# Kernel tuning notes

Measured on AMD Instinct MI355X. Metric: run time of the kernel, lower is better.

Reference implementation:

```python
import jax, jax.numpy as jnp
import numpy as np


def _relu(x):
    return jnp.maximum(x, 0.0)


def _wn(V, g):
    # torch weight_norm with dim=None: W = g * V / ||V||_F (scalar g)
    return g * V / jnp.linalg.norm(V)


def _wn_rank(V, g):
    # V: [rank, out, in], g: [rank] -> per-rank weight-normed weights
    n = jnp.sqrt(jnp.sum(V * V, axis=(1, 2), keepdims=True))
    return g[:, None, None] * V / n


def setup_inputs() -> dict:
    key = jax.random.key(0)
    ks = jax.random.split(key, 20)
    B, N, D, H, R, HK, G = 16, 64, 512, 512, 8, 64, 2
    f = lambda i, shape, s=1.0: jax.random.normal(ks[i], shape, dtype=jnp.float32) * s
    u = lambda i, shape: jax.random.uniform(ks[i], shape, dtype=jnp.float32)
    return {
        'v': f(0, (B, N, D)), 'q': f(1, (B, N, D)), 'a': f(2, (B, N, D)),
        'V_v': f(3, (H, D), 0.05), 'g_v': u(4, (1,)), 'b_v': f(5, (H,), 0.05),
        'V_q': f(6, (H, D), 0.05), 'g_q': u(7, (1,)), 'b_q': f(8, (H,), 0.05),
        'V_a': f(9, (H, D), 0.05), 'g_a': u(10, (1,)), 'b_a': f(11, (H,), 0.05),
        'Vn_v': f(12, (R, HK, H), 0.05), 'gn_v': u(13, (R,)), 'bn_v': f(14, (R, HK), 0.05),
        'Vn_qa': f(15, (R, HK, H), 0.05), 'gn_qa': u(16, (R,)), 'bn_qa': f(17, (R, HK), 0.05),
        'T_g': f(18, (R, HK, HK, HK, G), 0.02),  # T_g with h_out=1 squeezed
        'gamma': u(19, (H,)), 'beta': jnp.zeros((H,), jnp.float32),
    }


def reference(v, q, a, V_v, g_v, b_v, V_q, g_q, b_q, V_a, g_a, b_a,
              Vn_v, gn_v, bn_v, Vn_qa, gn_qa, bn_qa, T_g, gamma, beta):
    # Tucker projections (FCNet = weight-normed Linear + ReLU; dropout off in eval)
    v_t = _relu(v @ _wn(V_v, g_v).T + b_v)  # [B, Nv, H]
    q_t = _relu(q @ _wn(V_q, g_q).T + b_q)  # [B, Nq, H]
    a_t = _relu(a @ _wn(V_a, g_a).T + b_a)  # [B, Na, H]

    # Per-rank FCNets, vectorized over the rank loop (q_net and a_net share weights)
    Wv = _wn_rank(Vn_v, gn_v)    # [R, HK, H]
    Wqa = _wn_rank(Vn_qa, gn_qa)  # [R, HK, H]
    v_r = _relu(jnp.einsum('bnh,rkh->brnk', v_t, Wv) + bn_v[None, :, None, :])   # [B,R,Nv,HK]
    q_r = _relu(jnp.einsum('bnh,rkh->brnk', q_t, Wqa) + bn_qa[None, :, None, :])  # [B,R,Nq,HK]
    a_r = _relu(jnp.einsum('bnh,rkh->brnk', a_t, Wqa) + bn_qa[None, :, None, :])  # [B,R,Na,HK]

    # ModeProduct summed over rank: f_emb[b,v,q,m,g] = sum_r T_g[r,h,k,l,g] v_r q_r a_r
    t = jnp.einsum('brvh,rhklg->brvklg', v_r, T_g)
    t = jnp.einsum('brvklg,brqk->brvqlg', t, q_r)
    f_emb = jnp.einsum('brvqlg,brml->bvqmg', t, a_r)  # [B, Nv, Nq, Na, G]

    # logits = einsum('bdv,bvqag,bdqi,bdaj->bdijg').sum(-1).squeeze(3).squeeze(2)
    # with i=j=1 this is: logits[b,d] = sum_{v,q,a,g} v_t f_emb q_t a_t
    t2 = jnp.einsum('bvqag,bad->bvqdg', f_emb, a_t)
    t2 = jnp.einsum('bvqdg,bqd->bvdg', t2, q_t)
    logits = jnp.einsum('bvdg,bvd->bd', t2, v_t)  # [B, H]

    # BatchNorm1d (training-mode batch statistics, eps=1e-5)
    mu = jnp.mean(logits, axis=0)
    var = jnp.var(logits, axis=0)
    logits = (logits - mu) / jnp.sqrt(var + 1e-5) * gamma + beta

    # torch returns f_emb.squeeze(4): no-op since glimpse=2
    return f_emb, logits
```

## Files before the change

### kernel.cpp

```cpp
#include <hip/hip_runtime.h>
#include <hip/hip_fp16.h>
#include <math.h>


typedef _Float16 f16x8 __attribute__((ext_vector_type(8)));
typedef float f32x4 __attribute__((ext_vector_type(4)));

__device__ __forceinline__ unsigned short f2h(float x) {
  _Float16 h = (_Float16)x;
  return __builtin_bit_cast(unsigned short, h);
}

__device__ __forceinline__ int fragoff(int row, int kr) {
  return (((row & 15) + (((kr >> 2) & 3) << 4)) << 3) + (kr & 3) + (((kr >> 4) & 1) << 2);
}

#define WS_NRM 0
#define WS_VT  32
#define WS_QT  (WS_VT + 524288)
#define WS_AT  (WS_QT + 524288)
#define WS_LP  (WS_AT + 524288)
#define WS_LR  (WS_LP + 524288)
#define WS_PRT (WS_LR + 8192)
#define WS_H   (WS_PRT + 1280)
#define H_VRL 0
#define H_QR2 524288
#define H_AR2 1048576
#define H_T2  1572864
#define H_AT16 5767168
#define H_IN16 6291456
#define H_WB16 7864320
#define H_WN16 8650752
#define H_RP16 9175040

__global__ __launch_bounds__(256) void k_norms_part(
    const float* __restrict__ Vv, const float* __restrict__ Vq, const float* __restrict__ Va,
    const float* __restrict__ Vnv, const float* __restrict__ Vnqa, float* __restrict__ prt)
{
  const int bx = blockIdx.x;
  int n, j;
  const float* base;
  if (bx < 192) {
    n = bx >> 6; j = bx & 63;
    base = (n == 0 ? Vv : n == 1 ? Vq : Va) + j * 4096;
  } else {
    int t = bx - 192;
    n = 3 + (t >> 3); j = t & 7;
    base = (n < 11 ? Vnv + (n - 3) * 32768 : Vnqa + (n - 11) * 32768) + j * 4096;
  }
  const float4* p4 = (const float4*)base;
  float s = 0.f;
  #pragma unroll
  for (int i = 0; i < 4; ++i) {
    float4 x = p4[threadIdx.x + i * 256];
    s += x.x * x.x + x.y * x.y + x.z * x.z + x.w * x.w;
  }
  __shared__ float red[256];
  red[threadIdx.x] = s; __syncthreads();
  for (int off = 128; off > 0; off >>= 1) {
    if (threadIdx.x < off) red[threadIdx.x] += red[threadIdx.x + off];
    __syncthreads();
  }
  if (threadIdx.x == 0) prt[n * 64 + j] = red[0];
}

__global__ __launch_bounds__(64) void k_norms_fin(const float* __restrict__ prt, float* __restrict__ wsn)
{
  const int n = blockIdx.x, t = threadIdx.x;
  const int cnt = (n < 3) ? 64 : 8;
  float s = (t < cnt) ? prt[n * 64 + t] : 0.f;
  #pragma unroll
  for (int off = 32; off > 0; off >>= 1) s += __shfl_down(s, off);
  if (t == 0) wsn[n] = sqrtf(s);
}

__global__ __launch_bounds__(256) void k_inconv16(
    const float* __restrict__ v, const float* __restrict__ q, const float* __restrict__ a,
    unsigned short* __restrict__ IN16)
{
  const int z = blockIdx.y;
  const float4* src = (const float4*)((z == 0) ? v : (z == 1) ? q : a);
  #pragma unroll
  for (int i = 0; i < 8; ++i) {
    int f = blockIdx.x * 2048 + threadIdx.x + i * 256;
    int row = f >> 7, d0 = (f & 127) * 4;
    float4 x = src[f];
    ushort4 pk;
    pk.x = f2h(x.x); pk.y = f2h(x.y); pk.z = f2h(x.z); pk.w = f2h(x.w);
    int lanep = (row & 15) + (((d0 >> 2) & 3) << 4);
    int jb = ((d0 >> 4) & 1) << 2;
    size_t off = ((size_t)(z * 64 + (row >> 4)) * 16 + (d0 >> 5)) * 512 + lanep * 8 + jb;
    *(ushort4*)&IN16[off] = pk;
  }
}

__global__ __launch_bounds__(256) void k_wconv16(
    const float* __restrict__ Wv, const float* __restrict__ Wq, const float* __restrict__ Wa,
    const float* __restrict__ gv, const float* __restrict__ gq, const float* __restrict__ ga,
    const float* __restrict__ wsn, unsigned short* __restrict__ WB16)
{
  const int z = blockIdx.y;
  const float4* src = (const float4*)((z == 0) ? Wv : (z == 1) ? Wq : Wa);
  const float scale = ((z == 0) ? gv[0] : (z == 1) ? gq[0] : ga[0]) / wsn[z];
  #pragma unroll
  for (int i = 0; i < 8; ++i) {
    int f = blockIdx.x * 2048 + threadIdx.x + i * 256;
    int n = f >> 7, d0 = (f & 127) * 4;
    float4 x = src[f];
    ushort4 pk;
    pk.x = f2h(x.x * scale); pk.y = f2h(x.y * scale);
    pk.z = f2h(x.z * scale); pk.w = f2h(x.w * scale);
    int lanep = (n & 15) + (((d0 >> 2) & 3) << 4);
    int jb = ((d0 >> 4) & 1) << 2;
    size_t off = ((size_t)(z * 32 + (n >> 4)) * 16 + (d0 >> 5)) * 512 + lanep * 8 + jb;
    *(ushort4*)&WB16[off] = pk;
  }
}

__global__ __launch_bounds__(256) void k_wnconv16(
    const float* __restrict__ Vnv, const float* __restrict__ Vnqa,
    const float* __restrict__ gnv, const float* __restrict__ gnqa,
    const float* __restrict__ wsn, unsigned short* __restrict__ WN16)
{
  const int zr = blockIdx.x >> 2, sub = blockIdx.x & 3;
  const int zq = zr >> 3, r = zr & 7;
  const float4* src = (const float4*)((zq == 0 ? Vnv : Vnqa) + (size_t)r * 32768);
  const float scale = (zq == 0) ? (gnv[r] / wsn[3 + r]) : (gnqa[r] / wsn[11 + r]);
  #pragma unroll
  for (int i = 0; i < 8; ++i) {
    int f = sub * 2048 + threadIdx.x + i * 256;
    int n = f >> 7, d0 = (f & 127) * 4;
    float4 x = src[f];
    ushort4 pk;
    pk.x = f2h(x.x * scale); pk.y = f2h(x.y * scale);
    pk.z = f2h(x.z * scale); pk.w = f2h(x.w * scale);
    int lanep = (n & 15) + (((d0 >> 2) & 3) << 4);
    int jb = ((d0 >> 4) & 1) << 2;
    size_t off = ((size_t)(zr * 4 + (n >> 4)) * 16 + (d0 >> 5)) * 512 + lanep * 8 + jb;
    *(ushort4*)&WN16[off] = pk;
  }
}

__global__ __launch_bounds__(256) void k_repack2b(const float* __restrict__ Tg, unsigned short* __restrict__ T2)
{
  const int r = blockIdx.x >> 4, lB = blockIdx.x & 15;
  __shared__ unsigned short lds[32768];
  const int tid = threadIdx.x;

  #pragma unroll
  for (int i = 0; i < 32; ++i) {
    int f = tid + i * 256;
    int lpair = f & 1, k = (f >> 1) & 63, h = f >> 7;
    int l0 = lB * 4 + lpair * 2;
    const float4 x = *(const float4*)(Tg + ((size_t)((r * 64 + h) * 64 + k) * 64 + l0) * 2);
    const int el = fragoff(k & 15, h & 31);
    const int ks = h >> 5;
    const int ntr0 = (l0 & 3) * 4 + (k >> 4);
    const int ntr1 = ((l0 + 1) & 3) * 4 + (k >> 4);
    lds[((0 * 16 + ntr0) * 2 + ks) * 512 + el] = f2h(x.x);
    lds[((1 * 16 + ntr0) * 2 + ks) * 512 + el] = f2h(x.y);
    lds[((0 * 16 + ntr1) * 2 + ks) * 512 + el] = f2h(x.z);
    lds[((1 * 16 + ntr1) * 2 + ks) * 512 + el] = f2h(x.w);
  }
  __syncthreads();

  #pragma unroll
  for (int g = 0; g < 2; ++g) {
    unsigned short* dst = T2 + ((size_t)(g * 8 + r) * 256 + lB * 16) * 1024;
    const float4* s = (const float4*)&lds[g * 16384];
    float4* d = (float4*)dst;
    #pragma unroll
    for (int i = 0; i < 8; ++i) d[tid + i * 256] = s[tid + i * 256];
  }
}

__global__ __launch_bounds__(256) void k_proj16(
    const unsigned short* __restrict__ IN16, const unsigned short* __restrict__ WB16,
    const float* __restrict__ bv, const float* __restrict__ bq, const float* __restrict__ ba,
    float* __restrict__ ov, float* __restrict__ oq, float* __restrict__ oa,
    unsigned short* __restrict__ RP16, unsigned short* __restrict__ AT16)
{
  const int nB = blockIdx.x, mB = blockIdx.y, z = blockIdx.z;
  const float* bias = (z == 0) ? bv : (z == 1) ? bq : ba;
  float* out = (z == 0) ? ov : (z == 1) ? oq : oa;
  const int tid = threadIdx.x, lane = tid & 63;
  const int w = __builtin_amdgcn_readfirstlane(tid >> 6);

  f32x4 c[4];
  #pragma unroll
  for (int mt = 0; mt < 4; ++mt) c[mt] = (f32x4){0.f, 0.f, 0.f, 0.f};

  #pragma unroll 4
  for (int ks = 0; ks < 16; ++ks) {
    f16x8 af[4], bfr;
    #pragma unroll
    for (int mt = 0; mt < 4; ++mt)
      af[mt] = *(const f16x8*)&IN16[((size_t)(z * 64 + mB * 4 + mt) * 16 + ks) * 512 + lane * 8];
    bfr = *(const f16x8*)&WB16[((size_t)(z * 32 + nB * 4 + w) * 16 + ks) * 512 + lane * 8];
    #pragma unroll
    for (int mt = 0; mt < 4; ++mt)
      c[mt] = __builtin_amdgcn_mfma_f32_16x16x32_f16(af[mt], bfr, c[mt], 0, 0, 0);
  }

  const int col = nB * 64 + w * 16 + (lane & 15);
  const float bb = bias[col];
  #pragma unroll
  for (int mt = 0; mt < 4; ++mt)
    #pragma unroll
    for (int i = 0; i < 4; ++i) {
      const int row = mB * 64 + mt * 16 + 4 * (lane >> 4) + i;
      float val = fmaxf(c[mt][i] + bb, 0.f);
      unsigned short hv = f2h(val);
      out[(size_t)row * 512 + col] = val;
      RP16[((size_t)(z * 64 + (row >> 4)) * 16 + (col >> 5)) * 512 + fragoff(row, col & 31)] = hv;
      if (z == 2) {
        const int m = row & 63;
        AT16[(size_t)(row >> 6) * 32768 + ((col >> 4) * 2 + (m >> 5)) * 512 + fragoff(col & 15, m & 31)] = hv;
      }
    }
}

__global__ __launch_bounds__(256) void k_rproj16(
    const unsigned short* __restrict__ RP16, const unsigned short* __restrict__ WN16,
    const float* __restrict__ bnv, const float* __restrict__ bnqa,
    unsigned short* __restrict__ vrLin, unsigned short* __restrict__ qrT2,
    unsigned short* __restrict__ arT2)
{
  const int r = blockIdx.x, mB = blockIdx.y, z = blockIdx.z;
  const int zq = (z == 0) ? 0 : 1;
  const float* bias = ((z == 0) ? bnv : bnqa) + r * 64;
  const int tid = threadIdx.x, lane = tid & 63;
  const int w = __builtin_amdgcn_readfirstlane(tid >> 6);
  const int wm = w >> 1, wn = w & 1;

  f32x4 c[2][2];
  #pragma unroll
  for (int mi = 0; mi < 2; ++mi)
    #pragma unroll
    for (int ni = 0; ni < 2; ++ni) c[mi][ni] = (f32x4){0.f, 0.f, 0.f, 0.f};

  #pragma unroll 4
  for (int ks = 0; ks < 16; ++ks) {
    f16x8 af[2], bf[2];
    #pragma unroll
    for (int mi = 0; mi < 2; ++mi)
      af[mi] = *(const f16x8*)&RP16[((size_t)(z * 64 + mB * 4 + wm * 2 + mi) * 16 + ks) * 512 + lane * 8];
    #pragma unroll
    for (int ni = 0; ni < 2; ++ni)
      bf[ni] = *(const f16x8*)&WN16[((size_t)((zq * 8 + r) * 4 + wn * 2 + ni) * 16 + ks) * 512 + lane * 8];
    #pragma unroll
    for (int mi = 0; mi < 2; ++mi)
      #pragma unroll
      for (int ni = 0; ni < 2; ++ni)
        c[mi][ni] = __builtin_amdgcn_mfma_f32_16x16x32_f16(af[mi], bf[ni], c[mi][ni], 0, 0, 0);
  }

  #pragma unroll
  for (int mi = 0; mi < 2; ++mi)
    #pragma unroll
    for (int ni = 0; ni < 2; ++ni) {
      const int n = (wn * 2 + ni) * 16 + (lane & 15);
      const float bb2 = bias[n];
      #pragma unroll
      for (int i = 0; i < 4; ++i) {
        const int mm = mB * 64 + (wm * 2 + mi) * 16 + 4 * (lane >> 4) + i;
        const int bb = mm >> 6, nr = mm & 63;
        float val = fmaxf(c[mi][ni][i] + bb2, 0.f);
        unsigned short hv = f2h(val);
        if (z == 0)
          vrLin[((size_t)(bb * 8 + r) * 64 + nr) * 64 + n] = hv;
        else if (z == 1)
          qrT2[(size_t)(bb * 8 + r) * 4096 + ((nr >> 4) * 2 + (n >> 5)) * 512 + fragoff(nr, n & 31)] = hv;
        else
          arT2[(size_t)(((bb * 8 + r) * 2 + (n >> 5)) * 4 + (nr >> 4)) * 512 + fragoff(nr, n & 31)] = hv;
      }
    }
}

__global__ __launch_bounds__(512) void k_tucker16(
    const unsigned short* __restrict__ vrLin, const unsigned short* __restrict__ qrT2,
    const unsigned short* __restrict__ arT2, const unsigned short* __restrict__ T2,
    float* __restrict__ fout)
{
  const int b = blockIdx.x, vt = blockIdx.y, g = blockIdx.z;
  const int tid = threadIdx.x, lane = tid & 63;
  const int w = __builtin_amdgcn_readfirstlane(tid >> 6);

  __shared__ __align__(16) unsigned short UA[16384];
  __shared__ __align__(16) unsigned short QB[4096];
  __shared__ __align__(16) unsigned short AB[2048];
  __shared__ __align__(16) unsigned short CC[8192];
  __shared__ __align__(16) unsigned short VRL[512];

  f32x4 f[2][2][4];
  #pragma unroll
  for (int qh = 0; qh < 2; ++qh)
    #pragma unroll
    for (int qt = 0; qt < 2; ++qt)
      #pragma unroll
      for (int nt = 0; nt < 4; ++nt)
        f[qh][qt][nt] = (f32x4){0.f, 0.f, 0.f, 0.f};

  for (int r = 0; r < 8; ++r) {
    if (tid < 64)
      *(float4*)&VRL[tid * 8] =
          ((const float4*)(vrLin + (size_t)(b * 8 + r) * 4096 + vt * 512))[tid];
    *(float4*)&QB[tid * 8] = ((const float4*)(qrT2 + (size_t)(b * 8 + r) * 4096))[tid];
    __syncthreads();

    f16x8 af1[2];
    #pragma unroll
    for (int ks = 0; ks < 2; ++ks)
      #pragma unroll
      for (int j = 0; j < 8; ++j) {
        const int kr = (j & 3) + ((lane >> 4) & 3) * 4 + (j >> 2) * 16;
        af1[ks][j] = __builtin_bit_cast(_Float16, VRL[(lane & 7) * 64 + ks * 32 + kr]);
      }

    for (int lc = 0; lc < 2; ++lc) {
      if (tid < 256)
        ((float4*)AB)[tid] = ((const float4*)(arT2 + ((size_t)((b * 8 + r) * 2 + lc)) * 2048))[tid];

      const unsigned short* tb = T2 + ((size_t)((g * 8 + r) * 256 + lc * 128 + w * 16)) * 1024;
      for (int tg = 0; tg < 4; ++tg) {
        f16x8 bf[4][2];
        f32x4 d[4];
        #pragma unroll
        for (int tt = 0; tt < 4; ++tt) {
          #pragma unroll
          for (int ks = 0; ks < 2; ++ks)
            bf[tt][ks] = *(const f16x8*)&tb[(size_t)(tg * 4 + tt) * 1024 + ks * 512 + lane * 8];
          d[tt] = (f32x4){0.f, 0.f, 0.f, 0.f};
        }
        #pragma unroll
        for (int tt = 0; tt < 4; ++tt)
          #pragma unroll
          for (int ks = 0; ks < 2; ++ks)
            d[tt] = __builtin_amdgcn_mfma_f32_16x16x32_f16(af1[ks], bf[tt][ks], d[tt], 0, 0, 0);
        if (lane < 32) {
          #pragma unroll
          for (int tt = 0; tt < 4; ++tt) {
            const int t = w * 16 + tg * 4 + tt;
            const int lrel = t >> 2;
            const int k0 = (t & 3) * 16 + (lane & 15);
            #pragma unroll
            for (int i = 0; i < 4; ++i) {
              const int v = 4 * (lane >> 4) + i;
              const int row = lrel * 8 + v;
              UA[(row >> 4) * 1024 + (k0 >> 5) * 512 + fragoff(row & 15, k0 & 31)] = f2h(d[tt][i]);
            }
          }
        }
      }
      __syncthreads();

      f16x8 b3[4], a2[2][2];
      #pragma unroll
      for (int nt = 0; nt < 4; ++nt)
        b3[nt] = *(const f16x8*)&AB[nt * 512 + lane * 8];
      #pragma unroll
      for (int mi = 0; mi < 2; ++mi)
        #pragma unroll
        for (int ks = 0; ks < 2; ++ks)
          a2[mi][ks] = *(const f16x8*)&UA[(w * 2 + mi) * 1024 + ks * 512 + lane * 8];

      #pragma unroll
      for (int qh = 0; qh < 2; ++qh) {
        f32x4 c2[2][2];
        #pragma unroll
        for (int mi = 0; mi < 2; ++mi)
          #pragma unroll
          for (int nt = 0; nt < 2; ++nt)
            c2[mi][nt] = (f32x4){0.f, 0.f, 0.f, 0.f};

        f16x8 b2[2][2];
        #pragma unroll
        for (int nt = 0; nt < 2; ++nt)
          #pragma unroll
          for (int ks = 0; ks < 2; ++ks)
            b2[nt][ks] = *(const f16x8*)&QB[(qh * 2 + nt) * 1024 + ks * 512 + lane * 8];

        #pragma unroll
        for (int mi = 0; mi < 2; ++mi)
          #pragma unroll
          for (int nt = 0; nt < 2; ++nt)
            #pragma unroll
            for (int ks = 0; ks < 2; ++ks)
              c2[mi][nt] = __builtin_amdgcn_mfma_f32_16x16x32_f16(a2[mi][ks], b2[nt][ks], c2[mi][nt], 0, 0, 0);

        #pragma unroll
        for (int mi = 0; mi < 2; ++mi)
          #pragma unroll
          for (int nt = 0; nt < 2; ++nt)
            #pragma unroll
            for (int i = 0; i < 4; ++i) {
              const int row = (w * 2 + mi) * 16 + 4 * (lane >> 4) + i;
              const int l = row >> 3, v = row & 7;
              const int el = (v * 2 + nt) * 512 + fragoff(lane & 15, l);
              CC[el] = f2h(c2[mi][nt][i]);
            }
        __syncthreads();

        f16x8 a3[2];
        #pragma unroll
        for (int qt = 0; qt < 2; ++qt)
          a3[qt] = *(const f16x8*)&CC[(w * 2 + qt) * 512 + lane * 8];

        #pragma unroll
        for (int qt = 0; qt < 2; ++qt)
          #pragma unroll
          for (int nt = 0; nt < 4; ++nt)
            f[qh][qt][nt] = __builtin_amdgcn_mfma_f32_16x16x32_f16(a3[qt], b3[nt], f[qh][qt][nt], 0, 0, 0);
        __syncthreads();
      }
    }
  }

  #pragma unroll
  for (int qh = 0; qh < 2; ++qh)
    #pragma unroll
    for (int qt = 0; qt < 2; ++qt)
      #pragma unroll
      for (int nt = 0; nt < 4; ++nt)
        #pragma unroll
        for (int i = 0; i < 4; ++i) {
          const int q = qh * 32 + qt * 16 + 4 * (lane >> 4) + i;
          const int m = nt * 16 + (lane & 15);
          size_t addr = ((((size_t)b * 64 + vt * 8 + w) * 64 + q) * 64 + m) * 2 + g;
          fout[addr] = f[qh][qt][nt][i];
        }
}

__global__ __launch_bounds__(512) void k_logits2(
    const float* __restrict__ vt, const float* __restrict__ qt,
    const unsigned short* __restrict__ AT16, const float* __restrict__ fout,
    float* __restrict__ Lp)
{
  const int v = blockIdx.x, b = blockIdx.y;
  const int tid = threadIdx.x, lane = tid & 63;
  const int w = __builtin_amdgcn_readfirstlane(tid >> 6);

  __shared__ __align__(16) unsigned int FAu[2048];

  {
    const float4* fo4 = (const float4*)(fout + ((size_t)(b * 64 + v)) * 8192);
    #pragma unroll
    for (int i = 0; i < 4; ++i) {
      int fi = tid + i * 512;
      int q = fi >> 5, mpair = fi & 31;
      float4 x = fo4[fi];
      float s0 = x.x + x.y, s1 = x.z + x.w;
      int m0 = mpair * 2;
      int off = fragoff(q & 15, m0 & 31);
      int idx2 = (((q >> 4) * 2 + (m0 >> 5)) * 512 + off) >> 1;
      unsigned int pk = (unsigned int)f2h(s0) | ((unsigned int)f2h(s1) << 16);
      FAu[idx2] = pk;
    }
  }
  __syncthreads();

  const unsigned short* FAh = (const unsigned short*)FAu;

  f16x8 af[4][2], bf[4][2];
  #pragma unroll
  for (int mt = 0; mt < 4; ++mt)
    #pragma unroll
    for (int ks = 0; ks < 2; ++ks)
      af[mt][ks] = *(const f16x8*)&FAh[(mt * 2 + ks) * 512 + lane * 8];
  #pragma unroll
  for (int nt = 0; nt < 4; ++nt)
    #pragma unroll
    for (int ks = 0; ks < 2; ++ks)
      bf[nt][ks] = *(const f16x8*)&AT16[(size_t)((b * 32 + w * 4 + nt) * 2 + ks) * 512 + lane * 8];

  f32x4 c[4][4];
  #pragma unroll
  for (int mt = 0; mt < 4; ++mt)
    #pragma unroll
    for (int nt = 0; nt < 4; ++nt)
      c[mt][nt] = (f32x4){0.f, 0.f, 0.f, 0.f};

  #pragma unroll
  for (int mt = 0; mt < 4; ++mt)
    #pragma unroll
    for (int nt = 0; nt < 4; ++nt)
      #pragma unroll
      for (int ks = 0; ks < 2; ++ks)
        c[mt][nt] = __builtin_amdgcn_mfma_f32_16x16x32_f16(af[mt][ks], bf[nt][ks], c[mt][nt], 0, 0, 0);

  const int gr = lane >> 4, dl = lane & 15;
  #pragma unroll
  for (int nt = 0; nt < 4; ++nt) {
    const int d = w * 64 + nt * 16 + dl;
    float partial = 0.f;
    #pragma unroll
    for (int mt = 0; mt < 4; ++mt) {
      #pragma unroll
      for (int i = 0; i < 4; ++i) {
        const int q = mt * 16 + gr * 4 + i;
        partial += qt[(b * 64 + q) * 512 + d] * c[mt][nt][i];
      }
    }
    partial += __shfl_xor(partial, 16);
    partial += __shfl_xor(partial, 32);
    const float val = vt[(b * 64 + v) * 512 + d] * partial;
    if (lane < 16) Lp[((size_t)(b * 64 + v)) * 512 + d] = val;
  }
}

__global__ __launch_bounds__(512) void k_lred(const float* __restrict__ Lp, float* __restrict__ Lraw)
{
  const int b = blockIdx.x, d = threadIdx.x;
  float s = 0.f;
  for (int v = 0; v < 64; ++v) s += Lp[(size_t)(b * 64 + v) * 512 + d];
  Lraw[b * 512 + d] = s;
}

__global__ __launch_bounds__(512) void k_bn(
    const float* __restrict__ Lraw, const float* __restrict__ gamma,
    const float* __restrict__ beta, float* __restrict__ lout)
{
  const int d = threadIdx.x;
  float x[16]; float mu = 0.f;
  #pragma unroll
  for (int b = 0; b < 16; ++b) { x[b] = Lraw[b * 512 + d]; mu += x[b]; }
  mu *= (1.f / 16.f);
  float var = 0.f;
  #pragma unroll
  for (int b = 0; b < 16; ++b) { float t = x[b] - mu; var += t * t; }
  var *= (1.f / 16.f);
  const float sc = gamma[d] / sqrtf(var + 1e-5f);
  const float bt = beta[d];
  #pragma unroll
  for (int b = 0; b < 16; ++b) lout[b * 512 + d] = (x[b] - mu) * sc + bt;
}

extern "C" void kernel_launch(void* const* d_in, const int* in_sizes, int n_in,
                              void* d_out, int out_size, void* d_ws, size_t ws_size,
                              hipStream_t stream)
{
  const float* v    = (const float*)d_in[0];
  const float* q    = (const float*)d_in[1];
  const float* a    = (const float*)d_in[2];
  const float* Vv   = (const float*)d_in[3];
  const float* gv   = (const float*)d_in[4];
  const float* bv   = (const float*)d_in[5];
  const float* Vq   = (const float*)d_in[6];
  const float* gq   = (const float*)d_in[7];
  const float* bq   = (const float*)d_in[8];
  const float* Va   = (const float*)d_in[9];
  const float* ga   = (const float*)d_in[10];
  const float* ba   = (const float*)d_in[11];
  const float* Vnv  = (const float*)d_in[12];
  const float* gnv  = (const float*)d_in[13];
  const float* bnv  = (const float*)d_in[14];
  const float* Vnqa = (const float*)d_in[15];
  const float* gnqa = (const float*)d_in[16];
  const float* bnqa = (const float*)d_in[17];
  const float* Tg   = (const float*)d_in[18];
  const float* gamma= (const float*)d_in[19];
  const float* beta = (const float*)d_in[20];

  float* ws   = (float*)d_ws;
  unsigned short* hb = (unsigned short*)(ws + WS_H);
  float* fout = (float*)d_out;
  float* lout = fout + (size_t)16 * 64 * 64 * 64 * 2;

  k_norms_part<<<320, 256, 0, stream>>>(Vv, Vq, Va, Vnv, Vnqa, ws + WS_PRT);
  k_norms_fin<<<19, 64, 0, stream>>>(ws + WS_PRT, ws + WS_NRM);
  k_inconv16<<<dim3(64, 3), 256, 0, stream>>>(v, q, a, hb + H_IN16);
  k_wconv16<<<dim3(32, 3), 256, 0, stream>>>(Vv, Vq, Va, gv, gq, ga, ws + WS_NRM, hb + H_WB16);
  k_wnconv16<<<64, 256, 0, stream>>>(Vnv, Vnqa, gnv, gnqa, ws + WS_NRM, hb + H_WN16);
  k_repack2b<<<128, 256, 0, stream>>>(Tg, hb + H_T2);
  k_proj16<<<dim3(8, 16, 3), 256, 0, stream>>>(hb + H_IN16, hb + H_WB16, bv, bq, ba,
                                               ws + WS_VT, ws + WS_QT, ws + WS_AT,
                                               hb + H_RP16, hb + H_AT16);
  k_rproj16<<<dim3(8, 16, 3), 256, 0, stream>>>(hb + H_RP16, hb + H_WN16, bnv, bnqa,
                                                hb + H_VRL, hb + H_QR2, hb + H_AR2);
  k_tucker16<<<dim3(16, 8, 2), 512, 0, stream>>>(hb + H_VRL, hb + H_QR2, hb + H_AR2,
                                                 hb + H_T2, fout);
  k_logits2<<<dim3(64, 16), 512, 0, stream>>>(ws + WS_VT, ws + WS_QT,
                                              hb + H_AT16, fout, ws + WS_LP);
  k_lred<<<16, 512, 0, stream>>>(ws + WS_LP, ws + WS_LR);
  k_bn<<<1, 512, 0, stream>>>(ws + WS_LR, gamma, beta, lout);
}
```

Before: 156.7 us.

## Cut barriers in tucker kernel via double-buffered CC/AB and swizzled UA stores

The tucker kernel now loads both lc halves of the a-factor tile once per rank into a double-buffered shared array, instead of reloading per lc. CC is doubled so both qh halves are written before a single barrier, which removes two barriers per lc iteration. UA stores are spread across all 64 lanes, each half-wave handling two of the four tiles, instead of idling half the wave. A XOR swizzle is added to UA addressing to reduce LDS bank conflicts. Loops are also fully unrolled. The cost is more LDS use, which may lower occupancy, and higher register pressure from the unrolling.

```diff
diff --git a/kernel.cpp b/kernel.cpp
--- a/kernel.cpp
+++ b/kernel.cpp
@@ -13,6 +13,10 @@
 
 __device__ __forceinline__ int fragoff(int row, int kr) {
   return (((row & 15) + (((kr >> 2) & 3) << 4)) << 3) + (kr & 3) + (((kr >> 4) & 1) << 2);
+}
+
+__device__ __forceinline__ int swz(int h) {
+  return h ^ (((h >> 7) & 3) << 3);
 }
 
 #define WS_NRM 0
@@ -288,8 +292,8 @@
 
   __shared__ __align__(16) unsigned short UA[16384];
   __shared__ __align__(16) unsigned short QB[4096];
-  __shared__ __align__(16) unsigned short AB[2048];
-  __shared__ __align__(16) unsigned short CC[8192];
+  __shared__ __align__(16) unsigned short ABD[8192];
+  __shared__ __align__(16) unsigned short CC[16384];
   __shared__ __align__(16) unsigned short VRL[512];
 
   f32x4 f[2][2][4];
@@ -301,11 +305,15 @@
       for (int nt = 0; nt < 4; ++nt)
         f[qh][qt][nt] = (f32x4){0.f, 0.f, 0.f, 0.f};
 
+  const int half = lane >> 5;
+
   for (int r = 0; r < 8; ++r) {
+    *(float4*)&QB[tid * 8] = ((const float4*)(qrT2 + (size_t)(b * 8 + r) * 4096))[tid];
+    ((float4*)&ABD[(r & 1) * 4096])[tid] =
+        ((const float4*)(arT2 + (size_t)(b * 8 + r) * 4096))[tid];
     if (tid < 64)
       *(float4*)&VRL[tid * 8] =
           ((const float4*)(vrLin + (size_t)(b * 8 + r) * 4096 + vt * 512))[tid];
-    *(float4*)&QB[tid * 8] = ((const float4*)(qrT2 + (size_t)(b * 8 + r) * 4096))[tid];
     __syncthreads();
 
     f16x8 af1[2];
@@ -317,11 +325,10 @@
         af1[ks][j] = __builtin_bit_cast(_Float16, VRL[(lane & 7) * 64 + ks * 32 + kr]);
       }
 
+    #pragma unroll
     for (int lc = 0; lc < 2; ++lc) {
-      if (tid < 256)
-        ((float4*)AB)[tid] = ((const float4*)(arT2 + ((size_t)((b * 8 + r) * 2 + lc)) * 2048))[tid];
-
       const unsigned short* tb = T2 + ((size_t)((g * 8 + r) * 256 + lc * 128 + w * 16)) * 1024;
+      #pragma unroll
       for (int tg = 0; tg < 4; ++tg) {
         f16x8 bf[4][2];
         f32x4 d[4];
@@ -337,32 +344,29 @@
           #pragma unroll
           for (int ks = 0; ks < 2; ++ks)
             d[tt] = __builtin_amdgcn_mfma_f32_16x16x32_f16(af1[ks], bf[tt][ks], d[tt], 0, 0, 0);
-        if (lane < 32) {
-          #pragma unroll
-          for (int tt = 0; tt < 4; ++tt) {
-            const int t = w * 16 + tg * 4 + tt;
-            const int lrel = t >> 2;
-            const int k0 = (t & 3) * 16 + (lane & 15);
-            #pragma unroll
-            for (int i = 0; i < 4; ++i) {
-              const int v = 4 * (lane >> 4) + i;
-              const int row = lrel * 8 + v;
-              UA[(row >> 4) * 1024 + (k0 >> 5) * 512 + fragoff(row & 15, k0 & 31)] = f2h(d[tt][i]);
-            }
+        #pragma unroll
+        for (int tt2 = 0; tt2 < 2; ++tt2) {
+          const f32x4 dv = half ? d[tt2 + 2] : d[tt2];
+          const int t = w * 16 + tg * 4 + half * 2 + tt2;
+          const int lrel = t >> 2;
+          const int k0 = (t & 3) * 16 + (lane & 15);
+          #pragma unroll
+          for (int i = 0; i < 4; ++i) {
+            const int vv = 4 * ((lane >> 4) & 1) + i;
+            const int row = lrel * 8 + vv;
+            UA[(row >> 4) * 1024 + (k0 >> 5) * 512 + swz(fragoff(row & 15, k0 & 31))] =
+                f2h(dv[i]);
           }
         }
       }
       __syncthreads();
 
-      f16x8 b3[4], a2[2][2];
-      #pragma unroll
-      for (int nt = 0; nt < 4; ++nt)
-        b3[nt] = *(const f16x8*)&AB[nt * 512 + lane * 8];
+      f16x8 a2[2][2];
       #pragma unroll
       for (int mi = 0; mi < 2; ++mi)
         #pragma unroll
         for (int ks = 0; ks < 2; ++ks)
-          a2[mi][ks] = *(const f16x8*)&UA[(w * 2 + mi) * 1024 + ks * 512 + lane * 8];
+          a2[mi][ks] = *(const f16x8*)&UA[(w * 2 + mi) * 1024 + ks * 512 + swz(lane * 8)];
 
       #pragma unroll
       for (int qh = 0; qh < 2; ++qh) {
@@ -372,14 +376,12 @@
           #pragma unroll
           for (int nt = 0; nt < 2; ++nt)
             c2[mi][nt] = (f32x4){0.f, 0.f, 0.f, 0.f};
-
         f16x8 b2[2][2];
         #pragma unroll
         for (int nt = 0; nt < 2; ++nt)
           #pragma unroll
           for (int ks = 0; ks < 2; ++ks)
             b2[nt][ks] = *(const f16x8*)&QB[(qh * 2 + nt) * 1024 + ks * 512 + lane * 8];
-
         #pragma unroll
         for (int mi = 0; mi < 2; ++mi)
           #pragma unroll
@@ -387,7 +389,6 @@
             #pragma unroll
             for (int ks = 0; ks < 2; ++ks)
               c2[mi][nt] = __builtin_amdgcn_mfma_f32_16x16x32_f16(a2[mi][ks], b2[nt][ks], c2[mi][nt], 0, 0, 0);
-
         #pragma unroll
         for (int mi = 0; mi < 2; ++mi)
           #pragma unroll
@@ -396,22 +397,26 @@
             for (int i = 0; i < 4; ++i) {
               const int row = (w * 2 + mi) * 16 + 4 * (lane >> 4) + i;
               const int l = row >> 3, v = row & 7;
-              const int el = (v * 2 + nt) * 512 + fragoff(lane & 15, l);
-              CC[el] = f2h(c2[mi][nt][i]);
+              CC[qh * 8192 + (v * 2 + nt) * 512 + fragoff(lane & 15, l)] = f2h(c2[mi][nt][i]);
             }
-        __syncthreads();
-
+      }
+      __syncthreads();
+
+      f16x8 b3[4];
+      #pragma unroll
+      for (int nt = 0; nt < 4; ++nt)
+        b3[nt] = *(const f16x8*)&ABD[(r & 1) * 4096 + lc * 2048 + nt * 512 + lane * 8];
+      #pragma unroll
+      for (int qh = 0; qh < 2; ++qh) {
         f16x8 a3[2];
         #pragma unroll
         for (int qt = 0; qt < 2; ++qt)
-          a3[qt] = *(const f16x8*)&CC[(w * 2 + qt) * 512 + lane * 8];
-
+          a3[qt] = *(const f16x8*)&CC[qh * 8192 + (w * 2 + qt) * 512 + lane * 8];
         #pragma unroll
         for (int qt = 0; qt < 2; ++qt)
           #pragma unroll
           for (int nt = 0; nt < 4; ++nt)
             f[qh][qt][nt] = __builtin_amdgcn_mfma_f32_16x16x32_f16(a3[qt], b3[nt], f[qh][qt][nt], 0, 0, 0);
-        __syncthreads();
       }
     }
   }
```

Result: slower. 187.6 us (+19.7%).

## Split Tucker kernel over q halves across blocks to double grid parallelism

Applied to the files above, without the earlier changes.

The q dimension is split into two halves, each handled by its own block, doubling the tucker grid from 256 to 512 blocks. Each block now computes its own first mode product (v_r times T_g), so that stage is recomputed twice, while per-block accumulators and q-stage barriers are halved. The a_r tiles for both lc iterations are kept in separate shared buffers and the lc and tg loops are fully unrolled. The aim is better CU occupancy and fewer registers per block, traded against the duplicated T_g loads and MFMAs.

```diff
diff --git a/kernel.cpp b/kernel.cpp
--- a/kernel.cpp
+++ b/kernel.cpp
@@ -282,30 +282,31 @@
     const unsigned short* __restrict__ arT2, const unsigned short* __restrict__ T2,
     float* __restrict__ fout)
 {
-  const int b = blockIdx.x, vt = blockIdx.y, g = blockIdx.z;
+  const int b = blockIdx.x, vt = blockIdx.y;
+  const int g = blockIdx.z >> 1, qh = blockIdx.z & 1;
   const int tid = threadIdx.x, lane = tid & 63;
   const int w = __builtin_amdgcn_readfirstlane(tid >> 6);
 
   __shared__ __align__(16) unsigned short UA[16384];
-  __shared__ __align__(16) unsigned short QB[4096];
-  __shared__ __align__(16) unsigned short AB[2048];
+  __shared__ __align__(16) unsigned short QB[2048];
+  __shared__ __align__(16) unsigned short ABD[4096];
   __shared__ __align__(16) unsigned short CC[8192];
   __shared__ __align__(16) unsigned short VRL[512];
 
-  f32x4 f[2][2][4];
-  #pragma unroll
-  for (int qh = 0; qh < 2; ++qh)
-    #pragma unroll
-    for (int qt = 0; qt < 2; ++qt)
-      #pragma unroll
-      for (int nt = 0; nt < 4; ++nt)
-        f[qh][qt][nt] = (f32x4){0.f, 0.f, 0.f, 0.f};
+  f32x4 f[2][4];
+  #pragma unroll
+  for (int qt = 0; qt < 2; ++qt)
+    #pragma unroll
+    for (int nt = 0; nt < 4; ++nt)
+      f[qt][nt] = (f32x4){0.f, 0.f, 0.f, 0.f};
 
   for (int r = 0; r < 8; ++r) {
-    if (tid < 64)
-      *(float4*)&VRL[tid * 8] =
-          ((const float4*)(vrLin + (size_t)(b * 8 + r) * 4096 + vt * 512))[tid];
-    *(float4*)&QB[tid * 8] = ((const float4*)(qrT2 + (size_t)(b * 8 + r) * 4096))[tid];
+    if (tid < 256)
+      ((float4*)QB)[tid] =
+          ((const float4*)(qrT2 + (size_t)(b * 8 + r) * 4096 + qh * 2048))[tid];
+    else if (tid < 320)
+      ((float4*)VRL)[tid - 256] =
+          ((const float4*)(vrLin + (size_t)(b * 8 + r) * 4096 + vt * 512))[tid - 256];
     __syncthreads();
 
     f16x8 af1[2];
@@ -317,11 +318,14 @@
         af1[ks][j] = __builtin_bit_cast(_Float16, VRL[(lane & 7) * 64 + ks * 32 + kr]);
       }
 
+    #pragma unroll
     for (int lc = 0; lc < 2; ++lc) {
       if (tid < 256)
-        ((float4*)AB)[tid] = ((const float4*)(arT2 + ((size_t)((b * 8 + r) * 2 + lc)) * 2048))[tid];
+        ((float4*)&ABD[lc * 2048])[tid] =
+            ((const float4*)(arT2 + ((size_t)((b * 8 + r) * 2 + lc)) * 2048))[tid];
 
       const unsigned short* tb = T2 + ((size_t)((g * 8 + r) * 256 + lc * 128 + w * 16)) * 1024;
+      #pragma unroll
       for (int tg = 0; tg < 4; ++tg) {
         f16x8 bf[4][2];
         f32x4 d[4];
@@ -345,90 +349,80 @@
             const int k0 = (t & 3) * 16 + (lane & 15);
             #pragma unroll
             for (int i = 0; i < 4; ++i) {
-              const int v = 4 * (lane >> 4) + i;
-              const int row = lrel * 8 + v;
-              UA[(row >> 4) * 1024 + (k0 >> 5) * 512 + fragoff(row & 15, k0 & 31)] = f2h(d[tt][i]);
+              const int vv = 4 * (lane >> 4) + i;
+              const int row = lrel * 8 + vv;
+              UA[(row >> 4) * 1024 + (k0 >> 5) * 512 + fragoff(row & 15, k0 & 31)] =
+                  f2h(d[tt][i]);
             }
           }
         }
       }
       __syncthreads();
 
-      f16x8 b3[4], a2[2][2];
-      #pragma unroll
-      for (int nt = 0; nt < 4; ++nt)
-        b3[nt] = *(const f16x8*)&AB[nt * 512 + lane * 8];
+      f16x8 a2[2][2];
       #pragma unroll
       for (int mi = 0; mi < 2; ++mi)
         #pragma unroll
         for (int ks = 0; ks < 2; ++ks)
           a2[mi][ks] = *(const f16x8*)&UA[(w * 2 + mi) * 1024 + ks * 512 + lane * 8];
 
-      #pragma unroll
-      for (int qh = 0; qh < 2; ++qh) {
-        f32x4 c2[2][2];
-        #pragma unroll
-        for (int mi = 0; mi < 2; ++mi)
-          #pragma unroll
-          for (int nt = 0; nt < 2; ++nt)
-            c2[mi][nt] = (f32x4){0.f, 0.f, 0.f, 0.f};
-
-        f16x8 b2[2][2];
+      f32x4 c2[2][2];
+      #pragma unroll
+      for (int mi = 0; mi < 2; ++mi)
+        #pragma unroll
+        for (int nt = 0; nt < 2; ++nt)
+          c2[mi][nt] = (f32x4){0.f, 0.f, 0.f, 0.f};
+      f16x8 b2[2][2];
+      #pragma unroll
+      for (int nt = 0; nt < 2; ++nt)
+        #pragma unroll
+        for (int ks = 0; ks < 2; ++ks)
+          b2[nt][ks] = *(const f16x8*)&QB[nt * 1024 + ks * 512 + lane * 8];
+      #pragma unroll
+      for (int mi = 0; mi < 2; ++mi)
         #pragma unroll
         for (int nt = 0; nt < 2; ++nt)
           #pragma unroll
           for (int ks = 0; ks < 2; ++ks)
-            b2[nt][ks] = *(const f16x8*)&QB[(qh * 2 + nt) * 1024 + ks * 512 + lane * 8];
-
-        #pragma unroll
-        for (int mi = 0; mi < 2; ++mi)
+            c2[mi][nt] = __builtin_amdgcn_mfma_f32_16x16x32_f16(a2[mi][ks], b2[nt][ks], c2[mi][nt], 0, 0, 0);
+      #pragma unroll
+      for (int mi = 0; mi < 2; ++mi)
+        #pragma unroll
+        for (int nt = 0; nt < 2; ++nt)
           #pragma unroll
-          for (int nt = 0; nt < 2; ++nt)
-            #pragma unroll
-            for (int ks = 0; ks < 2; ++ks)
-              c2[mi][nt] = __builtin_amdgcn_mfma_f32_16x16x32_f16(a2[mi][ks], b2[nt][ks], c2[mi][nt], 0, 0, 0);
-
-        #pragma unroll
-        for (int mi = 0; mi < 2; ++mi)
-          #pragma unroll
-          for (int nt = 0; nt < 2; ++nt)
-            #pragma unroll
-            for (int i = 0; i < 4; ++i) {
-              const int row = (w * 2 + mi) * 16 + 4 * (lane >> 4) + i;
-              const int l = row >> 3, v = row & 7;
-              const int el = (v * 2 + nt) * 512 + fragoff(lane & 15, l);
-              CC[el] = f2h(c2[mi][nt][i]);
-            }
-        __syncthreads();
-
-        f16x8 a3[2];
-        #pragma unroll
-        for (int qt = 0; qt < 2; ++qt)
-          a3[qt] = *(const f16x8*)&CC[(w * 2 + qt) * 512 + lane * 8];
-
-        #pragma unroll
-        for (int qt = 0; qt < 2; ++qt)
-          #pragma unroll
-          for (int nt = 0; nt < 4; ++nt)
-            f[qh][qt][nt] = __builtin_amdgcn_mfma_f32_16x16x32_f16(a3[qt], b3[nt], f[qh][qt][nt], 0, 0, 0);
-        __syncthreads();
+          for (int i = 0; i < 4; ++i) {
+            const int row = (w * 2 + mi) * 16 + 4 * (lane >> 4) + i;
+            const int l = row >> 3, v = row & 7;
+            CC[(v * 2 + nt) * 512 + fragoff(lane & 15, l)] = f2h(c2[mi][nt][i]);
+          }
+      __syncthreads();
+
+      f16x8 b3[4], a3[2];
+      #pragma unroll
+      for (int nt = 0; nt < 4; ++nt)
+        b3[nt] = *(const f16x8*)&ABD[lc * 2048 + nt * 512 + lane * 8];
+      #pragma unroll
+      for (int qt = 0; qt < 2; ++qt)
+        a3[qt] = *(const f16x8*)&CC[(w * 2 + qt) * 512 + lane * 8];
+      #pragma unroll
+      for (int qt = 0; qt < 2; ++qt)
+        #pragma unroll
+        for (int nt = 0; nt < 4; ++nt)
+          f[qt][nt] = __builtin_amdgcn_mfma_f32_16x16x32_f16(a3[qt], b3[nt], f[qt][nt], 0, 0, 0);
+    }
+  }
+
+  #pragma unroll
+  for (int qt = 0; qt < 2; ++qt)
+    #pragma unroll
+    for (int nt = 0; nt < 4; ++nt)
+      #pragma unroll
+      for (int i = 0; i < 4; ++i) {
+        const int q = qh * 32 + qt * 16 + 4 * (lane >> 4) + i;
+        const int m = nt * 16 + (lane & 15);
+        size_t addr = ((((size_t)b * 64 + vt * 8 + w) * 64 + q) * 64 + m) * 2 + g;
+        fout[addr] = f[qt][nt][i];
       }
-    }
-  }
-
-  #pragma unroll
-  for (int qh = 0; qh < 2; ++qh)
-    #pragma unroll
-    for (int qt = 0; qt < 2; ++qt)
-      #pragma unroll
-      for (int nt = 0; nt < 4; ++nt)
-        #pragma unroll
-        for (int i = 0; i < 4; ++i) {
-          const int q = qh * 32 + qt * 16 + 4 * (lane >> 4) + i;
-          const int m = nt * 16 + (lane & 15);
-          size_t addr = ((((size_t)b * 64 + vt * 8 + w) * 64 + q) * 64 + m) * 2 + g;
-          fout[addr] = f[qh][qt][nt][i];
-        }
 }
 
 __global__ __launch_bounds__(512) void k_logits2(
@@ -577,7 +571,7 @@
                                                hb + H_RP16, hb + H_AT16);
   k_rproj16<<<dim3(8, 16, 3), 256, 0, stream>>>(hb + H_RP16, hb + H_WN16, bnv, bnqa,
                                                 hb + H_VRL, hb + H_QR2, hb + H_AR2);
-  k_tucker16<<<dim3(16, 8, 2), 512, 0, stream>>>(hb + H_VRL, hb + H_QR2, hb + H_AR2,
+  k_tucker16<<<dim3(16, 8, 4), 512, 0, stream>>>(hb + H_VRL, hb + H_QR2, hb + H_AR2,
                                                  hb + H_T2, fout);
   k_logits2<<<dim3(64, 16), 512, 0, stream>>>(ws + WS_VT, ws + WS_QT,
                                               hb + H_AT16, fout, ws + WS_LP);
```

New measurement: 184.1 us. 17.5% more time.
